# Kernel optimization log

Measured on AMD Instinct MI355X. Metric: run time of the kernel, lower is better.

The kernel has to match this reference:

```python
import jax, jax.numpy as jnp
import numpy as np

N, E, G = 100000, 3200000, 256
IN_C, HID = 3, 32


def setup_inputs() -> dict:
    key = jax.random.key(0)
    ks = jax.random.split(key, 10)
    x = jax.random.normal(ks[0], (N, IN_C), dtype=jnp.float32)
    edge_index = jax.random.randint(ks[1], (2, E), 0, N, dtype=jnp.int64)
    edge_weight = jax.random.uniform(ks[2], (E,), dtype=jnp.float32)
    batch = jnp.sort(jax.random.randint(ks[3], (N,), 0, G, dtype=jnp.int64))
    # GCNConv params (PyG: out = norm-agg(x @ W) + b), glorot-ish init
    W0 = jax.random.normal(ks[4], (IN_C, HID), dtype=jnp.float32) / np.sqrt(IN_C)
    b0 = jnp.zeros((HID,), dtype=jnp.float32)
    W1 = jax.random.normal(ks[5], (HID, HID), dtype=jnp.float32) / np.sqrt(HID)
    b1 = jnp.zeros((HID,), dtype=jnp.float32)
    Wr = jax.random.normal(ks[6], (HID, 1), dtype=jnp.float32) / np.sqrt(HID)
    br = jnp.zeros((1,), dtype=jnp.float32)
    return {"x": x, "edge_index": edge_index, "edge_weight": edge_weight,
            "batch": batch, "W0": W0, "b0": b0, "W1": W1, "b1": b1,
            "Wr": Wr, "br": br}


def _gcn_conv(x, row, col, w_edge, W, b, n_nodes):
    # PyG GCNConv with add_self_loops + symmetric normalization
    h = x @ W                                   # [N, H]
    deg = jax.ops.segment_sum(w_edge, col, num_segments=n_nodes)
    dinv = jnp.where(deg > 0, jax.lax.rsqrt(deg), 0.0)
    norm = dinv[row] * w_edge * dinv[col]       # [E+N]
    msg = h[row] * norm[:, None]                # gather + scale
    agg = jax.ops.segment_sum(msg, col, num_segments=n_nodes)
    return agg + b


def reference(x, edge_index, edge_weight, batch, W0, b0, W1, b1, Wr, br):
    n = x.shape[0]
    loop = jnp.arange(n, dtype=edge_index.dtype)
    row = jnp.concatenate([edge_index[0], loop])   # source (j)
    col = jnp.concatenate([edge_index[1], loop])   # target (i)
    w = jnp.concatenate([edge_weight, jnp.ones((n,), dtype=edge_weight.dtype)])

    h = jax.nn.relu(_gcn_conv(x, row, col, w, W0, b0, n))
    h = jax.nn.relu(_gcn_conv(h, row, col, w, W1, b1, n))

    # global_mean_pool over graphs
    ones = jnp.ones((n,), dtype=h.dtype)
    cnt = jax.ops.segment_sum(ones, batch, num_segments=G)
    summed = jax.ops.segment_sum(h, batch, num_segments=G)
    hg = summed / jnp.maximum(cnt, 1.0)[:, None]   # [G, H]
    return (hg @ Wr + br).squeeze(-1)              # [G]
```

## Files before the change

### kernel.cpp

```cpp
#include <hip/hip_runtime.h>
#include <hip/hip_fp16.h>


#define TPB 256
#define NBMAX 512
#define BSH 8
#define BSZ 256
#define CAP 9216
#define ST 1024
#define SV 16
#define STILE (ST * SV)

typedef unsigned long long u64;
union H8 { float4 f4; __half2 h2[4]; };
union HU { __half h; unsigned short u; };

__global__ void k_init(unsigned* cursor, float* gsum, float* gcnt, int nb, int g) {
    int t = threadIdx.x;
    for (int j = t; j < nb; j += blockDim.x) cursor[j] = 0u;
    for (int j = t; j < g; j += blockDim.x) { gsum[j] = 0.0f; gcnt[j] = 0.0f; }
}

__global__ void __launch_bounds__(1024) k_scat(const int* __restrict__ row,
                       const int* __restrict__ col, const float* __restrict__ w,
                       unsigned* cursor, int2* __restrict__ tmp, int nb, int e) {
    __shared__ unsigned cl[NBMAX];
    __shared__ unsigned bl[NBMAX];
    int t = threadIdx.x;
    for (int j = t; j < nb; j += ST) cl[j] = 0u;
    __syncthreads();
    const int4* c4 = (const int4*)col;
    int e4 = e >> 2;
    int base4 = blockIdx.x * (STILE >> 2);
    int4 cv[SV / 4];
    unsigned rk[SV];
    bool vld[SV / 4];
    #pragma unroll
    for (int v = 0; v < SV / 4; ++v) {
        int i4 = base4 + t + v * ST;
        vld[v] = (i4 < e4);
        if (vld[v]) {
            cv[v] = c4[i4];
            rk[4 * v + 0] = atomicAdd(&cl[cv[v].x >> BSH], 1u);
            rk[4 * v + 1] = atomicAdd(&cl[cv[v].y >> BSH], 1u);
            rk[4 * v + 2] = atomicAdd(&cl[cv[v].z >> BSH], 1u);
            rk[4 * v + 3] = atomicAdd(&cl[cv[v].w >> BSH], 1u);
        }
    }
    int tailc = -1; unsigned tailrk = 0; int taili = 0;
    if (blockIdx.x == 0) {
        int i = (e4 << 2) + t;
        if (i < e) { taili = i; tailc = col[i]; tailrk = atomicAdd(&cl[tailc >> BSH], 1u); }
    }
    __syncthreads();
    for (int j = t; j < nb; j += ST) {
        unsigned c = cl[j];
        bl[j] = c ? atomicAdd(&cursor[j], c) : 0u;
    }
    __syncthreads();
    const int4* r4 = (const int4*)row;
    const float4* w4 = (const float4*)w;
    #pragma unroll
    for (int v = 0; v < SV / 4; ++v) {
        if (vld[v]) {
            int i4 = base4 + t + v * ST;
            int4 rr = r4[i4];
            float4 ww = w4[i4];
            int c, b; unsigned lo;
            c = cv[v].x; b = c >> BSH; lo = bl[b] + rk[4 * v + 0];
            if (lo < CAP) tmp[(size_t)b * CAP + lo] =
                make_int2((int)(((unsigned)(c & 255) << 24) | (unsigned)rr.x), __float_as_int(ww.x));
            c = cv[v].y; b = c >> BSH; lo = bl[b] + rk[4 * v + 1];
            if (lo < CAP) tmp[(size_t)b * CAP + lo] =
                make_int2((int)(((unsigned)(c & 255) << 24) | (unsigned)rr.y), __float_as_int(ww.y));
            c = cv[v].z; b = c >> BSH; lo = bl[b] + rk[4 * v + 2];
            if (lo < CAP) tmp[(size_t)b * CAP + lo] =
                make_int2((int)(((unsigned)(c & 255) << 24) | (unsigned)rr.z), __float_as_int(ww.z));
            c = cv[v].w; b = c >> BSH; lo = bl[b] + rk[4 * v + 3];
            if (lo < CAP) tmp[(size_t)b * CAP + lo] =
                make_int2((int)(((unsigned)(c & 255) << 24) | (unsigned)rr.w), __float_as_int(ww.w));
        }
    }
    if (tailc >= 0) {
        int b = tailc >> BSH; unsigned lo = bl[b] + tailrk;
        if (lo < CAP) tmp[(size_t)b * CAP + lo] =
            make_int2((int)(((unsigned)(tailc & 255) << 24) | (unsigned)row[taili]),
                      __float_as_int(w[taili]));
    }
}

__global__ void __launch_bounds__(1024) k_conv(const int2* __restrict__ tmp,
                       const unsigned* __restrict__ cursor, unsigned* __restrict__ nodeinfo,
                       float* __restrict__ dinv, unsigned* __restrict__ arr, int n) {
    __shared__ unsigned cnt[BSZ];
    __shared__ float dw[BSZ];
    __shared__ unsigned cur[BSZ];
    int t = threadIdx.x, b = blockIdx.x;
    if (t < BSZ) { cnt[t] = 0u; dw[t] = 1.0f; }
    __syncthreads();
    unsigned cb = cursor[b]; if (cb > CAP) cb = CAP;
    size_t base = (size_t)b * CAP;
    for (unsigned k = t; k < cb; k += 1024) {
        int2 p = tmp[base + k];
        unsigned c = (unsigned)p.x >> 24;
        atomicAdd(&cnt[c], 1u);
        atomicAdd(&dw[c], __int_as_float(p.y));
    }
    __syncthreads();
    unsigned v = 0;
    if (t < BSZ) { v = cnt[t]; cur[t] = v; }
    __syncthreads();
    for (int off = 1; off < BSZ; off <<= 1) {
        unsigned u = (t < BSZ && t >= off) ? cur[t - off] : 0u;
        __syncthreads();
        if (t < BSZ) cur[t] += u;
        __syncthreads();
    }
    if (t < BSZ) {
        unsigned excl = cur[t] - v;
        int node = (b << BSH) + t;
        if (node < n) {
            unsigned cc = v > 1023u ? 1023u : v;
            nodeinfo[node] = (cc << 22) | (unsigned)(base + excl);
            dinv[node] = rsqrtf(dw[t]);
        }
        cur[t] = excl;
    }
    __syncthreads();
    for (unsigned k = t; k < cb; k += 1024) {
        int2 p = tmp[base + k];
        unsigned c = (unsigned)p.x >> 24;
        unsigned slot = atomicAdd(&cur[c], 1u);
        HU wu; wu.h = __float2half(__int_as_float(p.y));
        arr[base + slot] = ((unsigned)(wu.u & 0x7FFFu) << 17) | ((unsigned)p.x & 0x1FFFFu);
    }
}

__global__ void k_xw0(const float* __restrict__ x, const float* __restrict__ W0,
                      const float* __restrict__ dinv, float4* __restrict__ hw4, int n) {
    int t = blockIdx.x * blockDim.x + threadIdx.x;
    if (t >= n * 4) return;
    int i = t >> 2, q = t & 3;
    float x0 = x[i * 3 + 0], x1 = x[i * 3 + 1], x2 = x[i * 3 + 2];
    float di = dinv[i];
    int cb = q * 8;
    H8 u;
    #pragma unroll
    for (int j = 0; j < 4; ++j) {
        int c = cb + 2 * j;
        float a = di * (x0 * W0[c]     + x1 * W0[32 + c]     + x2 * W0[64 + c]);
        float b = di * (x0 * W0[c + 1] + x1 * W0[32 + c + 1] + x2 * W0[64 + c + 1]);
        u.h2[j] = __float22half2_rn(make_float2(a, b));
    }
    hw4[t] = u.f4;
}

#define EACC(V) { \
    unsigned rr_ = (V) & 0x1FFFFu; \
    HU wu_; wu_.u = (unsigned short)((V) >> 17); \
    float wv_ = __half2float(wu_.h); \
    H8 gA_, gB_; \
    gA_.f4 = tb[(size_t)rr_ << 2]; \
    gB_.f4 = tb[((size_t)rr_ << 2) + 1]; \
    float2 f_; \
    f_ = __half22float2(gA_.h2[0]); a[0] = fmaf(wv_, f_.x, a[0]); a[1] = fmaf(wv_, f_.y, a[1]); \
    f_ = __half22float2(gA_.h2[1]); a[2] = fmaf(wv_, f_.x, a[2]); a[3] = fmaf(wv_, f_.y, a[3]); \
    f_ = __half22float2(gA_.h2[2]); a[4] = fmaf(wv_, f_.x, a[4]); a[5] = fmaf(wv_, f_.y, a[5]); \
    f_ = __half22float2(gA_.h2[3]); a[6] = fmaf(wv_, f_.x, a[6]); a[7] = fmaf(wv_, f_.y, a[7]); \
    f_ = __half22float2(gB_.h2[0]); a[8] = fmaf(wv_, f_.x, a[8]); a[9] = fmaf(wv_, f_.y, a[9]); \
    f_ = __half22float2(gB_.h2[1]); a[10]= fmaf(wv_, f_.x, a[10]);a[11]= fmaf(wv_, f_.y, a[11]);\
    f_ = __half22float2(gB_.h2[2]); a[12]= fmaf(wv_, f_.x, a[12]);a[13]= fmaf(wv_, f_.y, a[13]);\
    f_ = __half22float2(gB_.h2[3]); a[14]= fmaf(wv_, f_.x, a[14]);a[15]= fmaf(wv_, f_.y, a[15]);}

#define EDGE_LOOP() { \
    for (; k + 4 <= hi; k += 4) { \
        unsigned v0 = __builtin_nontemporal_load(arr + k + 0); \
        unsigned v1 = __builtin_nontemporal_load(arr + k + 1); \
        unsigned v2 = __builtin_nontemporal_load(arr + k + 2); \
        unsigned v3 = __builtin_nontemporal_load(arr + k + 3); \
        EACC(v0) EACC(v1) EACC(v2) EACC(v3) \
    } \
    for (; k < hi; ++k) { \
        unsigned v = __builtin_nontemporal_load(arr + k); \
        EACC(v) \
    } }

__global__ void __launch_bounds__(256) k_agg1(const float4* __restrict__ tab4,
        const unsigned* __restrict__ arr, const unsigned* __restrict__ nodeinfo,
        const float* __restrict__ dinv, const float* __restrict__ W1,
        const float* __restrict__ b0, float4* __restrict__ out4, int n) {
    __shared__ float W1s[1024];
    __shared__ float b0s[32];
    __shared__ float hl[128 * 33];
    int tid = threadIdx.x;
    for (int j = tid; j < 1024; j += 256) W1s[j] = W1[j];
    if (tid < 32) b0s[tid] = b0[tid];
    int t = blockIdx.x * 256 + tid;
    int i = t >> 1, q = t & 1;
    if (i >= n) i = n - 1;
    int li = tid >> 1;
    unsigned info = nodeinfo[i];
    unsigned k = info & 0x3FFFFFu;
    unsigned hi = k + (info >> 22);
    const float4* tb = tab4 + (q << 1);
    float a[16];
    {
        H8 sA, sB;
        sA.f4 = tb[(size_t)i << 2];
        sB.f4 = tb[((size_t)i << 2) + 1];
        #pragma unroll
        for (int j = 0; j < 4; ++j) {
            float2 f0 = __half22float2(sA.h2[j]);
            float2 f1 = __half22float2(sB.h2[j]);
            a[2*j] = f0.x; a[2*j+1] = f0.y;
            a[8+2*j] = f1.x; a[8+2*j+1] = f1.y;
        }
    }
    EDGE_LOOP()
    float di = dinv[i];
    int cb = q << 4;
    float* hr = hl + li * 33;
    #pragma unroll
    for (int j = 0; j < 16; ++j)
        hr[cb + j] = fmaxf(di * a[j] + b0s[cb + j], 0.0f);
    __syncthreads();
    float o[16];
    #pragma unroll
    for (int j = 0; j < 16; ++j) o[j] = 0.0f;
    #pragma unroll
    for (int kk = 0; kk < 32; ++kk) {
        float hv = hr[kk];
        const float* wr = W1s + (kk << 5) + cb;
        #pragma unroll
        for (int j = 0; j < 16; ++j) o[j] = fmaf(hv, wr[j], o[j]);
    }
    H8 oA, oB;
    #pragma unroll
    for (int j = 0; j < 4; ++j) {
        oA.h2[j] = __float22half2_rn(make_float2(di * o[2*j],     di * o[2*j+1]));
        oB.h2[j] = __float22half2_rn(make_float2(di * o[8+2*j],   di * o[8+2*j+1]));
    }
    out4[((size_t)i << 2) + (q << 1)]     = oA.f4;
    out4[((size_t)i << 2) + (q << 1) + 1] = oB.f4;
}

__global__ void __launch_bounds__(256) k_agg2(const float4* __restrict__ tab4,
        const unsigned* __restrict__ arr, const unsigned* __restrict__ nodeinfo,
        const float* __restrict__ dinv, const float* __restrict__ b1,
        const float* __restrict__ Wr, const int* __restrict__ batch,
        float* gsum, float* gcnt, int n) {
    __shared__ float b1s[32];
    __shared__ float Wrs[32];
    int tid = threadIdx.x;
    if (tid < 32) { b1s[tid] = b1[tid]; Wrs[tid] = Wr[tid]; }
    __syncthreads();
    int t = blockIdx.x * 256 + tid;
    int i = t >> 1, q = t & 1;
    bool active = (i < n);
    int ii = active ? i : (n - 1);
    unsigned info = active ? nodeinfo[ii] : 0u;
    unsigned k = info & 0x3FFFFFu;
    unsigned hi = k + (info >> 22);
    const float4* tb = tab4 + (q << 1);
    float a[16];
    {
        H8 sA, sB;
        sA.f4 = tb[(size_t)ii << 2];
        sB.f4 = tb[((size_t)ii << 2) + 1];
        #pragma unroll
        for (int j = 0; j < 4; ++j) {
            float2 f0 = __half22float2(sA.h2[j]);
            float2 f1 = __half22float2(sB.h2[j]);
            a[2*j] = f0.x; a[2*j+1] = f0.y;
            a[8+2*j] = f1.x; a[8+2*j+1] = f1.y;
        }
    }
    EDGE_LOOP()
    float di = dinv[ii];
    int cb = q << 4;
    float sp = 0.0f;
    #pragma unroll
    for (int j = 0; j < 16; ++j)
        sp = fmaf(fmaxf(di * a[j] + b1s[cb + j], 0.0f), Wrs[cb + j], sp);
    if (!active) sp = 0.0f;
    sp += __shfl_xor(sp, 1);
    int bb = active ? batch[ii] : -1;
    int b0v = __shfl(bb, 0, 64);
    bool uniform = (b0v >= 0) && (__ballot(bb == b0v) == 0xFFFFFFFFFFFFFFFFULL);
    if (uniform) {
        float tot = (q == 0) ? sp : 0.0f;
        tot += __shfl_xor(tot, 1);
        tot += __shfl_xor(tot, 2);
        tot += __shfl_xor(tot, 4);
        tot += __shfl_xor(tot, 8);
        tot += __shfl_xor(tot, 16);
        tot += __shfl_xor(tot, 32);
        if ((tid & 63) == 0) {
            atomicAdd(&gsum[b0v], tot);
            atomicAdd(&gcnt[b0v], 32.0f);
        }
    } else if (active && q == 0) {
        atomicAdd(&gsum[bb], sp);
        atomicAdd(&gcnt[bb], 1.0f);
    }
}

__global__ void k_final(const float* gsum, const float* gcnt, const float* __restrict__ br,
                        float* out, int g) {
    int i = blockIdx.x * blockDim.x + threadIdx.x;
    if (i < g) out[i] = gsum[i] / fmaxf(gcnt[i], 1.0f) + br[0];
}

extern "C" void kernel_launch(void* const* d_in, const int* in_sizes, int n_in,
                              void* d_out, int out_size, void* d_ws, size_t ws_size,
                              hipStream_t stream) {
    const float* x     = (const float*)d_in[0];
    const int*   ei    = (const int*)d_in[1];
    const float* ew    = (const float*)d_in[2];
    const int*   batch = (const int*)d_in[3];
    const float* W0    = (const float*)d_in[4];
    const float* b0    = (const float*)d_in[5];
    const float* W1    = (const float*)d_in[6];
    const float* b1    = (const float*)d_in[7];
    const float* Wr    = (const float*)d_in[8];
    const float* br    = (const float*)d_in[9];
    float* out = (float*)d_out;

    int n = in_sizes[0] / 3;
    int e = in_sizes[2];
    int g = out_size;
    const int* row = ei;
    const int* col = ei + e;
    int nb = (n + BSZ - 1) >> BSH;

    char* ws = (char*)d_ws;
    size_t off = 0;
    auto alloc = [&](size_t bytes) -> void* {
        void* p = ws + off;
        off += (bytes + 255) & ~(size_t)255;
        return p;
    };
    unsigned* cursor   = (unsigned*)alloc((size_t)NBMAX * 4);
    unsigned* nodeinfo = (unsigned*)alloc((size_t)n * 4);
    float*    dinv     = (float*)   alloc((size_t)n * 4);
    float*    gsum     = (float*)   alloc((size_t)g * 4);
    float*    gcnt     = (float*)   alloc((size_t)g * 4);
    unsigned* arr      = (unsigned*)alloc((size_t)nb * CAP * 4);
    char*     region   = (char*)    alloc((size_t)nb * CAP * 8);
    int2*   tmp  = (int2*)region;
    float4* tab1 = (float4*)region;
    float4* tab2 = (float4*)(region + (size_t)n * 64);
    (void)ws_size;

    int stiles = (e + STILE - 1) / STILE;
    int nq4    = (n * 4 + TPB - 1) / TPB;
    int nq2    = (n * 2 + TPB - 1) / TPB;

    k_init  <<<1,      1024, 0, stream>>>(cursor, gsum, gcnt, nb, g);
    k_scat  <<<stiles, ST,   0, stream>>>(row, col, ew, cursor, tmp, nb, e);
    k_conv  <<<nb,     1024, 0, stream>>>(tmp, cursor, nodeinfo, dinv, arr, n);
    k_xw0   <<<nq4,    TPB,  0, stream>>>(x, W0, dinv, tab1, n);
    k_agg1  <<<nq2,    TPB,  0, stream>>>(tab1, arr, nodeinfo, dinv, W1, b0, tab2, n);
    k_agg2  <<<nq2,    TPB,  0, stream>>>(tab2, arr, nodeinfo, dinv, b1, Wr, batch, gsum, gcnt, n);
    k_final <<<1,      TPB,  0, stream>>>(gsum, gcnt, br, out, g);
}
```

Measured before the change: 288.2 us.

## Split feature tables into channel halves so each gather pass fits in cache

The 32-channel fp16 node tables are split into two 16-channel halves (3.2 MB each instead of 6.4 MB). Each aggregation layer now runs as two passes over the edge list, one per half, so the random gathers touch a smaller working set that is more likely to stay in L2/MALL. The cost is reading the edge array twice per layer, extra kernel launches, and an intermediate hA buffer for layer 1.

Result: slower. 363.3 us (+26.1%).

```diff
diff --git a/kernel.cpp b/kernel.cpp
--- a/kernel.cpp
+++ b/kernel.cpp
@@ -137,7 +137,8 @@
 }
 
 __global__ void k_xw0(const float* __restrict__ x, const float* __restrict__ W0,
-                      const float* __restrict__ dinv, float4* __restrict__ hw4, int n) {
+                      const float* __restrict__ dinv, float4* __restrict__ tabA,
+                      float4* __restrict__ tabB, int n) {
     int t = blockIdx.x * blockDim.x + threadIdx.x;
     if (t >= n * 4) return;
     int i = t >> 2, q = t & 3;
@@ -152,25 +153,20 @@
         float b = di * (x0 * W0[c + 1] + x1 * W0[32 + c + 1] + x2 * W0[64 + c + 1]);
         u.h2[j] = __float22half2_rn(make_float2(a, b));
     }
-    hw4[t] = u.f4;
+    if (q < 2) tabA[((size_t)i << 1) + q]       = u.f4;
+    else       tabB[((size_t)i << 1) + (q - 2)] = u.f4;
 }
 
 #define EACC(V) { \
     unsigned rr_ = (V) & 0x1FFFFu; \
     HU wu_; wu_.u = (unsigned short)((V) >> 17); \
     float wv_ = __half2float(wu_.h); \
-    H8 gA_, gB_; \
-    gA_.f4 = tb[(size_t)rr_ << 2]; \
-    gB_.f4 = tb[((size_t)rr_ << 2) + 1]; \
+    H8 g_; g_.f4 = tb[(size_t)rr_ << 1]; \
     float2 f_; \
-    f_ = __half22float2(gA_.h2[0]); a[0] = fmaf(wv_, f_.x, a[0]); a[1] = fmaf(wv_, f_.y, a[1]); \
-    f_ = __half22float2(gA_.h2[1]); a[2] = fmaf(wv_, f_.x, a[2]); a[3] = fmaf(wv_, f_.y, a[3]); \
-    f_ = __half22float2(gA_.h2[2]); a[4] = fmaf(wv_, f_.x, a[4]); a[5] = fmaf(wv_, f_.y, a[5]); \
-    f_ = __half22float2(gA_.h2[3]); a[6] = fmaf(wv_, f_.x, a[6]); a[7] = fmaf(wv_, f_.y, a[7]); \
-    f_ = __half22float2(gB_.h2[0]); a[8] = fmaf(wv_, f_.x, a[8]); a[9] = fmaf(wv_, f_.y, a[9]); \
-    f_ = __half22float2(gB_.h2[1]); a[10]= fmaf(wv_, f_.x, a[10]);a[11]= fmaf(wv_, f_.y, a[11]);\
-    f_ = __half22float2(gB_.h2[2]); a[12]= fmaf(wv_, f_.x, a[12]);a[13]= fmaf(wv_, f_.y, a[13]);\
-    f_ = __half22float2(gB_.h2[3]); a[14]= fmaf(wv_, f_.x, a[14]);a[15]= fmaf(wv_, f_.y, a[15]);}
+    f_ = __half22float2(g_.h2[0]); a[0] = fmaf(wv_, f_.x, a[0]); a[1] = fmaf(wv_, f_.y, a[1]); \
+    f_ = __half22float2(g_.h2[1]); a[2] = fmaf(wv_, f_.x, a[2]); a[3] = fmaf(wv_, f_.y, a[3]); \
+    f_ = __half22float2(g_.h2[2]); a[4] = fmaf(wv_, f_.x, a[4]); a[5] = fmaf(wv_, f_.y, a[5]); \
+    f_ = __half22float2(g_.h2[3]); a[6] = fmaf(wv_, f_.x, a[6]); a[7] = fmaf(wv_, f_.y, a[7]); }
 
 #define EDGE_LOOP() { \
     for (; k + 4 <= hi; k += 4) { \
@@ -185,106 +181,116 @@
         EACC(v) \
     } }
 
-__global__ void __launch_bounds__(256) k_agg1(const float4* __restrict__ tab4,
+#define AGG_PROLOG(TAB) \
+    int t = blockIdx.x * 256 + tid; \
+    int i = t >> 1, q = t & 1; \
+    bool active = (i < n); \
+    if (i >= n) i = n - 1; \
+    unsigned info = nodeinfo[i]; \
+    unsigned k = info & 0x3FFFFFu; \
+    unsigned hi = k + (info >> 22); \
+    const float4* tb = (TAB) + q; \
+    float a[8]; \
+    { H8 s_; s_.f4 = tb[(size_t)i << 1]; \
+      _Pragma("unroll") \
+      for (int j = 0; j < 4; ++j) { \
+          float2 f = __half22float2(s_.h2[j]); \
+          a[2*j] = f.x; a[2*j+1] = f.y; } } \
+    EDGE_LOOP()
+
+__global__ void __launch_bounds__(256) k_l1a(const float4* __restrict__ tabA,
         const unsigned* __restrict__ arr, const unsigned* __restrict__ nodeinfo,
-        const float* __restrict__ dinv, const float* __restrict__ W1,
-        const float* __restrict__ b0, float4* __restrict__ out4, int n) {
+        const float* __restrict__ dinv, const float* __restrict__ b0,
+        float4* __restrict__ hA, int n) {
+    __shared__ float b0s[16];
+    int tid = threadIdx.x;
+    if (tid < 16) b0s[tid] = b0[tid];
+    __syncthreads();
+    AGG_PROLOG(tabA)
+    float di = dinv[i];
+    int cb = q << 3;
+    H8 o;
+    #pragma unroll
+    for (int j = 0; j < 4; ++j) {
+        float v0 = fmaxf(di * a[2*j]   + b0s[cb + 2*j],     0.0f);
+        float v1 = fmaxf(di * a[2*j+1] + b0s[cb + 2*j + 1], 0.0f);
+        o.h2[j] = __float22half2_rn(make_float2(v0, v1));
+    }
+    hA[((size_t)i << 1) + q] = o.f4;
+}
+
+__global__ void __launch_bounds__(256) k_l1b(const float4* __restrict__ tabB,
+        const unsigned* __restrict__ arr, const unsigned* __restrict__ nodeinfo,
+        const float* __restrict__ dinv, const float* __restrict__ b0,
+        const float* __restrict__ W1, const float4* __restrict__ hA,
+        float4* __restrict__ tab2A, float4* __restrict__ tab2B, int n) {
     __shared__ float W1s[1024];
     __shared__ float b0s[32];
     __shared__ float hl[128 * 33];
     int tid = threadIdx.x;
     for (int j = tid; j < 1024; j += 256) W1s[j] = W1[j];
     if (tid < 32) b0s[tid] = b0[tid];
-    int t = blockIdx.x * 256 + tid;
-    int i = t >> 1, q = t & 1;
-    if (i >= n) i = n - 1;
+    __syncthreads();
+    AGG_PROLOG(tabB)
+    float di = dinv[i];
     int li = tid >> 1;
-    unsigned info = nodeinfo[i];
-    unsigned k = info & 0x3FFFFFu;
-    unsigned hi = k + (info >> 22);
-    const float4* tb = tab4 + (q << 1);
-    float a[16];
+    float* hr = hl + li * 33;
     {
-        H8 sA, sB;
-        sA.f4 = tb[(size_t)i << 2];
-        sB.f4 = tb[((size_t)i << 2) + 1];
+        int cb = 16 + (q << 3);
+        #pragma unroll
+        for (int j = 0; j < 8; ++j)
+            hr[cb + j] = fmaxf(di * a[j] + b0s[cb + j], 0.0f);
+        H8 ha; ha.f4 = hA[((size_t)i << 1) + q];
+        int ca = q << 3;
         #pragma unroll
         for (int j = 0; j < 4; ++j) {
-            float2 f0 = __half22float2(sA.h2[j]);
-            float2 f1 = __half22float2(sB.h2[j]);
-            a[2*j] = f0.x; a[2*j+1] = f0.y;
-            a[8+2*j] = f1.x; a[8+2*j+1] = f1.y;
-        }
-    }
-    EDGE_LOOP()
-    float di = dinv[i];
-    int cb = q << 4;
-    float* hr = hl + li * 33;
-    #pragma unroll
-    for (int j = 0; j < 16; ++j)
-        hr[cb + j] = fmaxf(di * a[j] + b0s[cb + j], 0.0f);
-    __syncthreads();
+            float2 f = __half22float2(ha.h2[j]);
+            hr[ca + 2*j] = f.x; hr[ca + 2*j + 1] = f.y;
+        }
+    }
+    __syncthreads();
+    int cb2 = q << 4;
     float o[16];
     #pragma unroll
     for (int j = 0; j < 16; ++j) o[j] = 0.0f;
     #pragma unroll
     for (int kk = 0; kk < 32; ++kk) {
         float hv = hr[kk];
-        const float* wr = W1s + (kk << 5) + cb;
+        const float* wr = W1s + (kk << 5) + cb2;
         #pragma unroll
         for (int j = 0; j < 16; ++j) o[j] = fmaf(hv, wr[j], o[j]);
     }
-    H8 oA, oB;
+    H8 o0, o1;
     #pragma unroll
     for (int j = 0; j < 4; ++j) {
-        oA.h2[j] = __float22half2_rn(make_float2(di * o[2*j],     di * o[2*j+1]));
-        oB.h2[j] = __float22half2_rn(make_float2(di * o[8+2*j],   di * o[8+2*j+1]));
-    }
-    out4[((size_t)i << 2) + (q << 1)]     = oA.f4;
-    out4[((size_t)i << 2) + (q << 1) + 1] = oB.f4;
-}
-
-__global__ void __launch_bounds__(256) k_agg2(const float4* __restrict__ tab4,
+        o0.h2[j] = __float22half2_rn(make_float2(di * o[2*j],     di * o[2*j+1]));
+        o1.h2[j] = __float22half2_rn(make_float2(di * o[8+2*j],   di * o[8+2*j+1]));
+    }
+    float4* dst = q ? tab2B : tab2A;
+    dst[((size_t)i << 1)]     = o0.f4;
+    dst[((size_t)i << 1) + 1] = o1.f4;
+}
+
+__global__ void __launch_bounds__(256) k_l2(const float4* __restrict__ tabH,
         const unsigned* __restrict__ arr, const unsigned* __restrict__ nodeinfo,
         const float* __restrict__ dinv, const float* __restrict__ b1,
         const float* __restrict__ Wr, const int* __restrict__ batch,
-        float* gsum, float* gcnt, int n) {
+        float* gsum, float* gcnt, int chbase, int do_cnt, int n) {
     __shared__ float b1s[32];
     __shared__ float Wrs[32];
     int tid = threadIdx.x;
     if (tid < 32) { b1s[tid] = b1[tid]; Wrs[tid] = Wr[tid]; }
     __syncthreads();
-    int t = blockIdx.x * 256 + tid;
-    int i = t >> 1, q = t & 1;
-    bool active = (i < n);
-    int ii = active ? i : (n - 1);
-    unsigned info = active ? nodeinfo[ii] : 0u;
-    unsigned k = info & 0x3FFFFFu;
-    unsigned hi = k + (info >> 22);
-    const float4* tb = tab4 + (q << 1);
-    float a[16];
-    {
-        H8 sA, sB;
-        sA.f4 = tb[(size_t)ii << 2];
-        sB.f4 = tb[((size_t)ii << 2) + 1];
-        #pragma unroll
-        for (int j = 0; j < 4; ++j) {
-            float2 f0 = __half22float2(sA.h2[j]);
-            float2 f1 = __half22float2(sB.h2[j]);
-            a[2*j] = f0.x; a[2*j+1] = f0.y;
-            a[8+2*j] = f1.x; a[8+2*j+1] = f1.y;
-        }
-    }
-    EDGE_LOOP()
-    float di = dinv[ii];
-    int cb = q << 4;
+    AGG_PROLOG(tabH)
+    float di = dinv[i];
+    int cb = chbase + (q << 3);
     float sp = 0.0f;
     #pragma unroll
-    for (int j = 0; j < 16; ++j)
+    for (int j = 0; j < 8; ++j)
         sp = fmaf(fmaxf(di * a[j] + b1s[cb + j], 0.0f), Wrs[cb + j], sp);
     if (!active) sp = 0.0f;
     sp += __shfl_xor(sp, 1);
-    int bb = active ? batch[ii] : -1;
+    int bb = active ? batch[i] : -1;
     int b0v = __shfl(bb, 0, 64);
     bool uniform = (b0v >= 0) && (__ballot(bb == b0v) == 0xFFFFFFFFFFFFFFFFULL);
     if (uniform) {
@@ -297,11 +303,11 @@
         tot += __shfl_xor(tot, 32);
         if ((tid & 63) == 0) {
             atomicAdd(&gsum[b0v], tot);
-            atomicAdd(&gcnt[b0v], 32.0f);
+            if (do_cnt) atomicAdd(&gcnt[b0v], 32.0f);
         }
     } else if (active && q == 0) {
         atomicAdd(&gsum[bb], sp);
-        atomicAdd(&gcnt[bb], 1.0f);
+        if (do_cnt) atomicAdd(&gcnt[bb], 1.0f);
     }
 }
 
@@ -347,9 +353,13 @@
     float*    gcnt     = (float*)   alloc((size_t)g * 4);
     unsigned* arr      = (unsigned*)alloc((size_t)nb * CAP * 4);
     char*     region   = (char*)    alloc((size_t)nb * CAP * 8);
-    int2*   tmp  = (int2*)region;
-    float4* tab1 = (float4*)region;
-    float4* tab2 = (float4*)(region + (size_t)n * 64);
+    size_t na = (((size_t)n * 32) + 255) & ~(size_t)255;
+    int2*   tmp   = (int2*)region;
+    float4* tab1A = (float4*)(region);
+    float4* tab1B = (float4*)(region + na);
+    float4* hA    = (float4*)(region + 2 * na);
+    float4* tab2A = (float4*)(region + 3 * na);
+    float4* tab2B = (float4*)(region + 4 * na);
     (void)ws_size;
 
     int stiles = (e + STILE - 1) / STILE;
@@ -359,8 +369,10 @@
     k_init  <<<1,      1024, 0, stream>>>(cursor, gsum, gcnt, nb, g);
     k_scat  <<<stiles, ST,   0, stream>>>(row, col, ew, cursor, tmp, nb, e);
     k_conv  <<<nb,     1024, 0, stream>>>(tmp, cursor, nodeinfo, dinv, arr, n);
-    k_xw0   <<<nq4,    TPB,  0, stream>>>(x, W0, dinv, tab1, n);
-    k_agg1  <<<nq2,    TPB,  0, stream>>>(tab1, arr, nodeinfo, dinv, W1, b0, tab2, n);
-    k_agg2  <<<nq2,    TPB,  0, stream>>>(tab2, arr, nodeinfo, dinv, b1, Wr, batch, gsum, gcnt, n);
+    k_xw0   <<<nq4,    TPB,  0, stream>>>(x, W0, dinv, tab1A, tab1B, n);
+    k_l1a   <<<nq2,    TPB,  0, stream>>>(tab1A, arr, nodeinfo, dinv, b0, hA, n);
+    k_l1b   <<<nq2,    TPB,  0, stream>>>(tab1B, arr, nodeinfo, dinv, b0, W1, hA, tab2A, tab2B, n);
+    k_l2    <<<nq2,    TPB,  0, stream>>>(tab2A, arr, nodeinfo, dinv, b1, Wr, batch, gsum, gcnt, 0,  1, n);
+    k_l2    <<<nq2,    TPB,  0, stream>>>(tab2B, arr, nodeinfo, dinv, b1, Wr, batch, gsum, gcnt, 16, 0, n);
     k_final <<<1,      TPB,  0, stream>>>(gsum, gcnt, br, out, g);
 }
```
